# Kernel optimization log

Measured on AMD Instinct MI355X. Metric: run time of the kernel, lower is better.

## Reference

```python
import jax, jax.numpy as jnp
import numpy as np

SAMP_RATE = 24000
UPSAMPLE = 300
HARMONIC_NUM = 8
DIM = HARMONIC_NUM + 1
SINE_AMP = 0.1
NOISE_STD = 0.003
VOICED_THRESHOLD = 0.0


def setup_inputs() -> dict:
    key = jax.random.key(0)
    k1, k2 = jax.random.split(key)
    B, L = 32, 120000  # L = 400 frames * UPSAMPLE
    # realistic f0 range [0, 400) Hz; voiced_threshold=0 so >0 is voiced
    f0 = jax.random.uniform(k1, (B, L, 1), dtype=jnp.float32) * 400.0
    noise = jax.random.normal(k2, (B, L, DIM), dtype=jnp.float32)
    return {"f0": f0, "noise": noise}


def reference(f0, noise):
    # f0: (B, L, 1), noise: (B, L, DIM) unit-normal
    uv = (f0 > VOICED_THRESHOLD).astype(jnp.float32)  # (B, L, 1)
    harmonics = jnp.arange(1, DIM + 1, dtype=jnp.float32)
    rad = (f0 * harmonics[None, None, :] / SAMP_RATE) % 1.0  # (B, L, DIM)
    # rand_ini is identically zero because f0 has one channel (rand_ini[:,0]=0)
    rad_t = jnp.transpose(rad, (0, 2, 1))  # (B, DIM, L)
    rad_ds = rad_t[..., ::UPSAMPLE]        # (B, DIM, F)  frame-rate phase increments
    phase = jnp.cumsum(rad_ds, axis=-1) * (2.0 * jnp.pi)  # (B, DIM, F)
    B, D, F = phase.shape
    # vectorized linear interpolation of phase between consecutive frames
    j = jnp.arange(UPSAMPLE, dtype=jnp.float32)
    slope = (phase[..., 1:] - phase[..., :-1]) / UPSAMPLE          # (B, DIM, F-1)
    seg = phase[..., :-1, None] + slope[..., None] * j             # (B, DIM, F-1, up)
    interp = seg.reshape(B, D, (F - 1) * UPSAMPLE)
    last = jnp.broadcast_to(phase[..., -1:], (B, D, UPSAMPLE))     # hold last frame
    phase_up = jnp.concatenate([interp, last], axis=-1)            # (B, DIM, L)
    sines = jnp.sin(jnp.transpose(phase_up, (0, 2, 1)))            # (B, L, DIM)
    sine_waves = sines * SINE_AMP
    noise_amp = uv * NOISE_STD + (1.0 - uv) * SINE_AMP / 3.0       # (B, L, 1)
    noise_scaled = noise_amp * noise                               # (B, L, DIM)
    sine_waves = sine_waves * uv + noise_scaled
    return (sine_waves, uv, noise_scaled)
```

## Files before the change

### kernel.cpp

```cpp
#include <hip/hip_runtime.h>
#include <math.h>

#define L_LEN     120000
#define BATCH     32
#define DIM       9
#define UPS       300
#define F_LEN     400
#define NCHAIN    (BATCH * DIM)
#define N_SINE    (BATCH * L_LEN * DIM)
#define N_UV      (BATCH * L_LEN)
#define TWO_PI_F  6.28318530717958647692f

__global__ __launch_bounds__(64) void phase_scan_kernel(
    const float* __restrict__ f0, float* __restrict__ phase)
{
    const int chain = blockIdx.x;
    const int b = chain / DIM;
    const int d = chain - b * DIM;
    const float h = (float)(d + 1);
    const int lane = threadIdx.x;
    const float* f0b = f0 + (size_t)b * L_LEN;
    float* pout = phase + (size_t)chain * F_LEN;

    float running = 0.0f;
    #pragma unroll
    for (int c = 0; c < 7; ++c) {
        const int idx = c * 64 + lane;
        float v = 0.0f;
        if (idx < F_LEN) {
            const float r = f0b[idx * UPS] * h / 24000.0f;
            v = r - floorf(r);
        }
        #pragma unroll
        for (int off = 1; off < 64; off <<= 1) {
            const float u = __shfl_up(v, off, 64);
            if (lane >= off) v += u;
        }
        const float ph = running + v;
        if (idx < F_LEN) pout[idx] = ph * TWO_PI_F;
        running += __shfl(v, 63, 64);
    }
}

__global__ __launch_bounds__(256) void sine_main_kernel(
    const float* __restrict__ f0, const float* __restrict__ noise,
    const float* __restrict__ phase, float* __restrict__ out_sine,
    float* __restrict__ out_uv, float* __restrict__ out_noise)
{
    const unsigned tid  = blockIdx.x * 256u + threadIdx.x;
    const unsigned base = tid * 4u;

    const float4 nin = *reinterpret_cast<const float4*>(noise + base);
    const float nel[4] = {nin.x, nin.y, nin.z, nin.w};
    float sv[4], nv[4];

    #pragma unroll
    for (int e = 0; e < 4; ++e) {
        const unsigned t  = base + (unsigned)e;
        const unsigned bl = t / 9u;
        const unsigned d  = t - bl * 9u;
        const unsigned b  = bl / 120000u;
        const unsigned l  = bl - b * 120000u;
        const unsigned f  = l / 300u;
        const unsigned j  = l - f * 300u;

        const float f0v  = f0[bl];
        const bool voiced = (f0v > 0.0f);
        const float uvf  = voiced ? 1.0f : 0.0f;
        const float namp = voiced ? 0.003f : (0.1f / 3.0f);

        const float* pb = phase + (size_t)((b * 9u + d) * 400u);
        float ph;
        if (f < 399u) {
            const float p0 = pb[f];
            const float p1 = pb[f + 1u];
            ph = p0 + ((p1 - p0) / 300.0f) * (float)j;
        } else {
            ph = pb[399];
        }

        const float s  = sinf(ph) * 0.1f;
        const float nz = namp * nel[e];
        sv[e] = s * uvf + nz;
        nv[e] = nz;
        if (d == 0u) out_uv[bl] = uvf;
    }

    *reinterpret_cast<float4*>(out_sine + base)  = make_float4(sv[0], sv[1], sv[2], sv[3]);
    *reinterpret_cast<float4*>(out_noise + base) = make_float4(nv[0], nv[1], nv[2], nv[3]);
}

extern "C" void kernel_launch(void* const* d_in, const int* in_sizes, int n_in,
                              void* d_out, int out_size, void* d_ws, size_t ws_size,
                              hipStream_t stream)
{
    const float* f0    = (const float*)d_in[0];
    const float* noise = (const float*)d_in[1];
    float* out         = (float*)d_out;

    float* out_sine  = out;
    float* out_uv    = out + N_SINE;
    float* out_noise = out + N_SINE + N_UV;

    float* phase = (float*)d_ws;

    phase_scan_kernel<<<NCHAIN, 64, 0, stream>>>(f0, phase);

    const int nthreads = N_SINE / 4;
    sine_main_kernel<<<nthreads / 256, 256, 0, stream>>>(
        f0, noise, phase, out_sine, out_uv, out_noise);
}
```

Baseline: 426.0 us.

## Split uv output into own kernel, use nontemporal IO and incremental indices

Moves the uv output writes into a separate vectorized kernel so they become coalesced float4 stores instead of scattered scalar stores inside the main kernel. The main kernel now uses nontemporal loads and stores for the streaming noise and outputs. It also computes the index divisions once per thread and advances the indices step by step across the four elements, and it multiplies by a reciprocal instead of dividing. This adds an extra kernel launch and reads f0 a second time.

```diff
diff --git a/kernel.cpp b/kernel.cpp
--- a/kernel.cpp
+++ b/kernel.cpp
@@ -10,6 +10,8 @@
 #define N_SINE    (BATCH * L_LEN * DIM)
 #define N_UV      (BATCH * L_LEN)
 #define TWO_PI_F  6.28318530717958647692f
+
+typedef float fx4 __attribute__((ext_vector_type(4)));
 
 __global__ __launch_bounds__(64) void phase_scan_kernel(
     const float* __restrict__ f0, float* __restrict__ phase)
@@ -42,29 +44,44 @@
     }
 }
 
+__global__ __launch_bounds__(256) void uv_kernel(
+    const float* __restrict__ f0, float* __restrict__ out_uv)
+{
+    const unsigned tid  = blockIdx.x * 256u + threadIdx.x;
+    const unsigned base = tid * 4u;
+    const fx4 fv = *reinterpret_cast<const fx4*>(f0 + base);
+    fx4 uv;
+    uv.x = (fv.x > 0.0f) ? 1.0f : 0.0f;
+    uv.y = (fv.y > 0.0f) ? 1.0f : 0.0f;
+    uv.z = (fv.z > 0.0f) ? 1.0f : 0.0f;
+    uv.w = (fv.w > 0.0f) ? 1.0f : 0.0f;
+    __builtin_nontemporal_store(uv, reinterpret_cast<fx4*>(out_uv + base));
+}
+
 __global__ __launch_bounds__(256) void sine_main_kernel(
     const float* __restrict__ f0, const float* __restrict__ noise,
     const float* __restrict__ phase, float* __restrict__ out_sine,
-    float* __restrict__ out_uv, float* __restrict__ out_noise)
+    float* __restrict__ out_noise)
 {
     const unsigned tid  = blockIdx.x * 256u + threadIdx.x;
     const unsigned base = tid * 4u;
 
-    const float4 nin = *reinterpret_cast<const float4*>(noise + base);
+    unsigned bl = base / 9u;
+    unsigned d  = base - bl * 9u;
+    unsigned b  = bl / 120000u;
+    unsigned l  = bl - b * 120000u;
+    unsigned f  = l / 300u;
+    unsigned j  = l - f * 300u;
+
+    float f0v = f0[bl];
+
+    const fx4 nin = __builtin_nontemporal_load(
+        reinterpret_cast<const fx4*>(noise + base));
     const float nel[4] = {nin.x, nin.y, nin.z, nin.w};
     float sv[4], nv[4];
 
     #pragma unroll
     for (int e = 0; e < 4; ++e) {
-        const unsigned t  = base + (unsigned)e;
-        const unsigned bl = t / 9u;
-        const unsigned d  = t - bl * 9u;
-        const unsigned b  = bl / 120000u;
-        const unsigned l  = bl - b * 120000u;
-        const unsigned f  = l / 300u;
-        const unsigned j  = l - f * 300u;
-
-        const float f0v  = f0[bl];
         const bool voiced = (f0v > 0.0f);
         const float uvf  = voiced ? 1.0f : 0.0f;
         const float namp = voiced ? 0.003f : (0.1f / 3.0f);
@@ -74,7 +91,7 @@
         if (f < 399u) {
             const float p0 = pb[f];
             const float p1 = pb[f + 1u];
-            ph = p0 + ((p1 - p0) / 300.0f) * (float)j;
+            ph = p0 + ((p1 - p0) * (1.0f / 300.0f)) * (float)j;
         } else {
             ph = pb[399];
         }
@@ -83,11 +100,20 @@
         const float nz = namp * nel[e];
         sv[e] = s * uvf + nz;
         nv[e] = nz;
-        if (d == 0u) out_uv[bl] = uvf;
+
+        ++d;
+        if (d == 9u) {
+            d = 0u; ++bl; ++l; ++j;
+            if (j == 300u) { j = 0u; ++f; }
+            if (l == 120000u) { ++b; l = 0u; f = 0u; j = 0u; }
+            f0v = f0[bl];
+        }
     }
 
-    *reinterpret_cast<float4*>(out_sine + base)  = make_float4(sv[0], sv[1], sv[2], sv[3]);
-    *reinterpret_cast<float4*>(out_noise + base) = make_float4(nv[0], nv[1], nv[2], nv[3]);
+    fx4 svv; svv.x = sv[0]; svv.y = sv[1]; svv.z = sv[2]; svv.w = sv[3];
+    fx4 nvv; nvv.x = nv[0]; nvv.y = nv[1]; nvv.z = nv[2]; nvv.w = nv[3];
+    __builtin_nontemporal_store(svv, reinterpret_cast<fx4*>(out_sine + base));
+    __builtin_nontemporal_store(nvv, reinterpret_cast<fx4*>(out_noise + base));
 }
 
 extern "C" void kernel_launch(void* const* d_in, const int* in_sizes, int n_in,
@@ -105,8 +131,7 @@
     float* phase = (float*)d_ws;
 
     phase_scan_kernel<<<NCHAIN, 64, 0, stream>>>(f0, phase);
-
-    const int nthreads = N_SINE / 4;
-    sine_main_kernel<<<nthreads / 256, 256, 0, stream>>>(
-        f0, noise, phase, out_sine, out_uv, out_noise);
+    uv_kernel<<<N_UV / 4 / 256, 256, 0, stream>>>(f0, out_uv);
+    sine_main_kernel<<<N_SINE / 4 / 256, 256, 0, stream>>>(
+        f0, noise, phase, out_sine, out_noise);
 }
```

New measurement: 422.5 us. Within noise of the previous version (-0.8%).
